# Kernel optimization log

Measured on AMD Instinct MI355X. Metric: run time of the kernel, lower is better.

Reference implementation:

```python
import jax, jax.numpy as jnp
import numpy as np

FACTOR = 5

def setup_inputs() -> dict:
    key = jax.random.key(0)
    kq, kk, kv, ki = jax.random.split(key, 4)
    B, L, H, D = 8, 2048, 8, 64
    u = FACTOR * int(np.ceil(np.log(L)))  # sample_k == n_top == 40
    return {
        "queries": jax.random.normal(kq, (B, L, H, D), dtype=jnp.float32),
        "keys": jax.random.normal(kk, (B, L, H, D), dtype=jnp.float32),
        "values": jax.random.normal(kv, (B, L, H, D), dtype=jnp.float32),
        "index_sample": jax.random.randint(ki, (L, u), 0, L, dtype=jnp.int32),
    }

def reference(queries, keys, values, index_sample):
    B, L, H, D = queries.shape
    # faithful to torch .view(B, H, -1, D) on contiguous tensors (a reshape, not a transpose)
    q = queries.reshape(B, H, L, D)
    k = keys.reshape(B, H, L, D)
    v = values.reshape(B, H, L, D)
    u = FACTOR * int(np.ceil(np.log(L)))  # U_part == u
    # --- _prob_QK: sample keys per query, score, pick top-u queries ---
    K_sample = k[:, :, index_sample, :]                      # [B,H,L,u,D] gather over L_K
    QK_sample = jnp.einsum('bhld,bhlsd->bhls', q, K_sample)  # [B,H,L,u]
    M = QK_sample.max(axis=-1) - QK_sample.sum(axis=-1) / L  # sparsity measure [B,H,L]
    M_top = jax.lax.top_k(M, u)[1]                           # [B,H,u] indices of active queries
    Q_reduce = jnp.take_along_axis(q, M_top[..., None], axis=2)  # [B,H,u,D]
    scores = jnp.einsum('bhud,bhld->bhul', Q_reduce, k)      # [B,H,u,L]
    scale = 1.0 / float(np.sqrt(D))
    attn = jax.nn.softmax(scores * scale, axis=-1)           # dropout is identity in eval
    context = jnp.einsum('bhul,bhld->bhud', attn, v)         # [B,H,u,D]
    return context, attn
```

## Files before the change

kernel.cpp:

```cpp
#include <hip/hip_runtime.h>
#include <math.h>

#define LSEQ 2048
#define DDIM 64
#define UU   40
#define NBH  64
#define NCHUNK 8
#define CROWS  256
#define CTX_ELEMS (NBH*UU*DDIM)

__device__ __forceinline__ float grp8_sum(float x) {
  float t;
  t = __int_as_float(__builtin_amdgcn_update_dpp(0, __float_as_int(x), 0xB1, 0xF, 0xF, false));
  x += t;
  t = __int_as_float(__builtin_amdgcn_update_dpp(0, __float_as_int(x), 0x4E, 0xF, 0xF, false));
  x += t;
  t = __int_as_float(__builtin_amdgcn_update_dpp(0, __float_as_int(x), 0x141, 0xF, 0xF, false));
  x += t;
  return x;
}

__global__ __launch_bounds__(256) void k0_sort(
    const int* __restrict__ idxs, int* __restrict__ sidx, int* __restrict__ soff) {
  int l = blockIdx.x * 4 + (threadIdx.x >> 6);
  int lane = threadIdx.x & 63;
  int v = 0, c = NCHUNK;
  if (lane < UU) { v = idxs[l * UU + lane]; c = v >> 8; }
  unsigned long long lower = (1ull << lane) - 1ull;
  int base = 0;
#pragma unroll
  for (int cc = 0; cc < NCHUNK; ++cc) {
    unsigned long long m = __ballot(c == cc);
    if (c == cc) {
      int rank = __popcll(m & lower);
      sidx[l * UU + base + rank] = v;
    }
    int cnt = __popcll(m);
    if (lane == cc) soff[l * NCHUNK + cc] = (base << 8) | cnt;
    base += cnt;
  }
}

__global__ __launch_bounds__(512, 4) void k12_gather(
    const float* __restrict__ q, const float* __restrict__ k,
    const int* __restrict__ sidx, const int* __restrict__ soff,
    float2* __restrict__ Mpart) {
  __shared__ float4 kt[CROWS * 16];
  int b = blockIdx.x;
  int bh = b & 63;
  int c  = b >> 6;
  int t  = threadIdx.x;

  {
    const float4* src = (const float4*)(k + ((size_t)bh * LSEQ + c * CROWS) * DDIM);
#pragma unroll
    for (int j = 0; j < 8; ++j) {
      int i = t + 512 * j;
      int row = i >> 4, col = i & 15;
      kt[row * 16 + (col ^ (row & 7))] = src[i];
    }
  }
  __syncthreads();

  int w = t >> 6;
  int lane = t & 63;
  int g = lane >> 3;
  int sub = lane & 7;

  for (int lb = 0; lb < 256; lb += 8) {
    int l = w * 256 + lb + g;
    const float4* qr = (const float4*)(q + ((size_t)bh * LSEQ + l) * DDIM);
    float4 qa = qr[sub];
    float4 qb = qr[sub + 8];
    int oc   = soff[l * NCHUNK + c];
    int cnt  = oc & 255;
    int base = oc >> 8;
    int rowv[8];
#pragma unroll
    for (int s = 0; s < 8; ++s) {
      int ix = base + s; ix = ix < UU ? ix : UU - 1;
      rowv[s] = sidx[l * UU + ix] & (CROWS - 1);
    }
    float mx = -INFINITY, sm = 0.f;
#pragma unroll
    for (int s = 0; s < 8; ++s) {
      if (s < cnt) {
        int row = rowv[s];
        int sl = (sub ^ (row & 7));
        float4 a  = kt[row * 16 + sl];
        float4 bq = kt[row * 16 + 8 + sl];
        float d = qa.x * a.x + qa.y * a.y + qa.z * a.z + qa.w * a.w
                + qb.x * bq.x + qb.y * bq.y + qb.z * bq.z + qb.w * bq.w;
        d = grp8_sum(d);
        mx = fmaxf(mx, d);
        sm += d;
      }
    }
    for (int s = 8; s < cnt; ++s) {
      int row = sidx[l * UU + base + s] & (CROWS - 1);
      int sl = (sub ^ (row & 7));
      float4 a  = kt[row * 16 + sl];
      float4 bq = kt[row * 16 + 8 + sl];
      float d = qa.x * a.x + qa.y * a.y + qa.z * a.z + qa.w * a.w
              + qb.x * bq.x + qb.y * bq.y + qb.z * bq.z + qb.w * bq.w;
      d = grp8_sum(d);
      mx = fmaxf(mx, d);
      sm += d;
    }
    if (sub == 0) Mpart[((size_t)bh * NCHUNK + c) * LSEQ + l] = make_float2(mx, sm);
  }
}

__global__ __launch_bounds__(256) void k3_topk(const float2* __restrict__ Mp,
                                               int* __restrict__ Mtop) {
  int bh = blockIdx.x;
  int t = threadIdx.x;
  int w = t >> 6;
  int lane = t & 63;
  float v[8];
#pragma unroll
  for (int j = 0; j < 8; ++j) {
    int l = t + 256 * j;
    float mxv = -INFINITY, smv = 0.f;
#pragma unroll
    for (int c = 0; c < NCHUNK; ++c) {
      float2 p = Mp[((size_t)bh * NCHUNK + c) * LSEQ + l];
      mxv = fmaxf(mxv, p.x);
      smv += p.y;
    }
    v[j] = mxv - smv * (1.0f / (float)LSEQ);
  }
  __shared__ float swv[4];
  __shared__ int   swi[4];
  __shared__ int   win;
  for (int it = 0; it < UU; ++it) {
    float bv = -INFINITY; int bi = 0x7fffffff;
#pragma unroll
    for (int j = 0; j < 8; ++j) {
      if (v[j] > bv) { bv = v[j]; bi = t + 256 * j; }
    }
#pragma unroll
    for (int off = 32; off > 0; off >>= 1) {
      float ov = __shfl_xor(bv, off, 64);
      int   oi = __shfl_xor(bi, off, 64);
      if (ov > bv || (ov == bv && oi < bi)) { bv = ov; bi = oi; }
    }
    if (lane == 0) { swv[w] = bv; swi[w] = bi; }
    __syncthreads();
    if (t == 0) {
      float fv = swv[0]; int fi = swi[0];
#pragma unroll
      for (int j = 1; j < 4; ++j) {
        if (swv[j] > fv || (swv[j] == fv && swi[j] < fi)) { fv = swv[j]; fi = swi[j]; }
      }
      Mtop[bh * UU + it] = fi;
      win = fi;
    }
    __syncthreads();
    int wi = win;
#pragma unroll
    for (int j = 0; j < 8; ++j)
      if (wi == t + 256 * j) v[j] = -INFINITY;
  }
}

__global__ __launch_bounds__(256, 4) void k45_scores_softmax(
    const float* __restrict__ q, const float* __restrict__ k,
    const int* __restrict__ Mtop, float* __restrict__ attn,
    float* __restrict__ ctx) {
  __shared__ float sct[4 * LSEQ];
  int b = blockIdx.x;
  int bh = b & 63;
  int u0 = (b >> 6) * 4;
  int t = threadIdx.x;
  int g = t >> 2;
  int sub = t & 3;

  ctx[b * 256 + t] = 0.f;

  float4 qv[4][4];
#pragma unroll
  for (int u = 0; u < 4; ++u) {
    int qi = Mtop[bh * UU + u0 + u];
    const float4* qr = (const float4*)(q + (size_t)(bh * LSEQ + qi) * DDIM);
#pragma unroll
    for (int m = 0; m < 4; ++m) qv[u][m] = qr[4 * m + sub];
  }

  const float* kb = k + (size_t)bh * LSEQ * DDIM;
#pragma unroll 1
  for (int p = 0; p < 32; ++p) {
    int l = p * 64 + g;
    const float4* kr = (const float4*)(kb + (size_t)l * DDIM);
    float4 ks[4];
#pragma unroll
    for (int m = 0; m < 4; ++m) ks[m] = kr[4 * m + sub];
    float d[4];
#pragma unroll
    for (int u = 0; u < 4; ++u) {
      float s = 0.f;
#pragma unroll
      for (int m = 0; m < 4; ++m) {
        float4 x = qv[u][m], a = ks[m];
        s += x.x * a.x + x.y * a.y + x.z * a.z + x.w * a.w;
      }
      s += __shfl_xor(s, 1, 64);
      s += __shfl_xor(s, 2, 64);
      d[u] = s * 0.125f;
    }
    if (sub == 0) {
#pragma unroll
      for (int u = 0; u < 4; ++u) sct[u * LSEQ + l] = d[u];
    }
  }
  __syncthreads();

  int w = t >> 6, lane = t & 63;
  float* row = sct + w * LSEQ;
  float vv[32];
  float mx = -INFINITY;
#pragma unroll
  for (int j = 0; j < 32; ++j) { vv[j] = row[lane + 64 * j]; mx = fmaxf(mx, vv[j]); }
#pragma unroll
  for (int off = 32; off > 0; off >>= 1) mx = fmaxf(mx, __shfl_xor(mx, off, 64));
  float sm = 0.f;
#pragma unroll
  for (int j = 0; j < 32; ++j) { vv[j] = __expf(vv[j] - mx); sm += vv[j]; }
#pragma unroll
  for (int off = 32; off > 0; off >>= 1) sm += __shfl_xor(sm, off, 64);
  float inv = 1.0f / sm;
  float* ap = attn + (size_t)(bh * UU + u0 + w) * LSEQ;
#pragma unroll
  for (int j = 0; j < 32; ++j) ap[lane + 64 * j] = vv[j] * inv;
}

__global__ __launch_bounds__(256) void k7_context(
    const float* __restrict__ attn, const float* __restrict__ v,
    float* __restrict__ ctx) {
  __shared__ float vt[256 * DDIM];
  int b = blockIdx.x;
  int bh = b & 63;
  int l0 = (b >> 6) * 256;
  int t = threadIdx.x;

  const float4* src = (const float4*)(v + ((size_t)bh * LSEQ + l0) * DDIM);
  float4* dst = (float4*)vt;
#pragma unroll
  for (int i = 0; i < 16; ++i) dst[t + 256 * i] = src[t + 256 * i];
  __syncthreads();

  int w = t >> 6;
  int d = t & 63;
  const float* ab = attn + ((size_t)bh * UU + w * 10) * LSEQ + l0;
  float acc[10];
#pragma unroll
  for (int u = 0; u < 10; ++u) acc[u] = 0.f;
#pragma unroll 1
  for (int l4 = 0; l4 < 64; ++l4) {
    int l = l4 * 4;
    float4 av[10];
#pragma unroll
    for (int u = 0; u < 10; ++u)
      av[u] = *(const float4*)(ab + (size_t)u * LSEQ + l);
#pragma unroll
    for (int i = 0; i < 4; ++i) {
      float vvv = vt[(l + i) * DDIM + d];
#pragma unroll
      for (int u = 0; u < 10; ++u)
        acc[u] = fmaf(((const float*)&av[u])[i], vvv, acc[u]);
    }
  }
#pragma unroll
  for (int u = 0; u < 10; ++u)
    atomicAdd(&ctx[((size_t)bh * UU + w * 10 + u) * DDIM + d], acc[u]);
}

extern "C" void kernel_launch(void* const* d_in, const int* in_sizes, int n_in,
                              void* d_out, int out_size, void* d_ws, size_t ws_size,
                              hipStream_t stream) {
  const float* q   = (const float*)d_in[0];
  const float* k   = (const float*)d_in[1];
  const float* v   = (const float*)d_in[2];
  const int*   idx = (const int*)d_in[3];

  float* ctx  = (float*)d_out;
  float* attn = (float*)d_out + CTX_ELEMS;
  float2* Mpart = (float2*)attn;

  int* sidx = (int*)d_ws;
  int* soff = sidx + LSEQ * UU;
  int* Mtop = soff + LSEQ * NCHUNK;

  k0_sort<<<LSEQ / 4, 256, 0, stream>>>(idx, sidx, soff);
  k12_gather<<<NBH * NCHUNK, 512, 0, stream>>>(q, k, sidx, soff, Mpart);
  k3_topk<<<NBH, 256, 0, stream>>>(Mpart, Mtop);
  k45_scores_softmax<<<NBH * 10, 256, 0, stream>>>(q, k, Mtop, attn, ctx);
  k7_context<<<NBH * 8, 256, 0, stream>>>(attn, v, ctx);
}
```

Measured before the change: 301.4 us.

## Fuse scores, softmax and context kernels, keeping attention in LDS

Merges the scores/softmax kernel with the context kernel. Each block keeps its 4 normalized attention rows in shared memory and streams V through a swizzled LDS tile to compute the context directly. This drops one launch, the re-read of attention from global memory and the ctx atomics, and the final per-row sum is done through shared memory. In exchange, each of the 640 blocks now reads the whole V for its head instead of a 256-row slice, giving about 10x total V traffic, and the launch bound drops from 4 to 3 blocks per SM.

New measurement: 290.5 us. -3.6%, faster.

```diff
diff --git a/kernel.cpp b/kernel.cpp
--- a/kernel.cpp
+++ b/kernel.cpp
@@ -164,115 +164,140 @@
   }
 }
 
-__global__ __launch_bounds__(256, 4) void k45_scores_softmax(
+__global__ __launch_bounds__(256, 3) void k457_fused(
     const float* __restrict__ q, const float* __restrict__ k,
-    const int* __restrict__ Mtop, float* __restrict__ attn,
-    float* __restrict__ ctx) {
-  __shared__ float sct[4 * LSEQ];
+    const float* __restrict__ v, const int* __restrict__ Mtop,
+    float* __restrict__ attn, float* __restrict__ ctx) {
+  __shared__ float  sct[4 * LSEQ];
+  __shared__ float4 vt4[64 * 16];
   int b = blockIdx.x;
   int bh = b & 63;
   int u0 = (b >> 6) * 4;
   int t = threadIdx.x;
-  int g = t >> 2;
-  int sub = t & 3;
-
-  ctx[b * 256 + t] = 0.f;
-
-  float4 qv[4][4];
+
+  {
+    int g = t >> 2;
+    int sub = t & 3;
+    float4 qv[4][4];
+#pragma unroll
+    for (int u = 0; u < 4; ++u) {
+      int qi = Mtop[bh * UU + u0 + u];
+      const float4* qr = (const float4*)(q + (size_t)(bh * LSEQ + qi) * DDIM);
+#pragma unroll
+      for (int m = 0; m < 4; ++m) qv[u][m] = qr[4 * m + sub];
+    }
+    const float* kb = k + (size_t)bh * LSEQ * DDIM;
+#pragma unroll 1
+    for (int p = 0; p < 32; ++p) {
+      int l = p * 64 + g;
+      const float4* kr = (const float4*)(kb + (size_t)l * DDIM);
+      float4 ks[4];
+#pragma unroll
+      for (int m = 0; m < 4; ++m) ks[m] = kr[4 * m + sub];
+      float d[4];
+#pragma unroll
+      for (int u = 0; u < 4; ++u) {
+        float s = 0.f;
+#pragma unroll
+        for (int m = 0; m < 4; ++m) {
+          float4 x = qv[u][m], a = ks[m];
+          s += x.x * a.x + x.y * a.y + x.z * a.z + x.w * a.w;
+        }
+        s += __shfl_xor(s, 1, 64);
+        s += __shfl_xor(s, 2, 64);
+        d[u] = s * 0.125f;
+      }
+      if (sub == 0) {
+#pragma unroll
+        for (int u = 0; u < 4; ++u) sct[u * LSEQ + l] = d[u];
+      }
+    }
+  }
+  __syncthreads();
+
+  int w = t >> 6, lane = t & 63;
+  {
+    float* row = sct + w * LSEQ;
+    float vv[32];
+    float mx = -INFINITY;
+#pragma unroll
+    for (int j = 0; j < 32; ++j) { vv[j] = row[lane + 64 * j]; mx = fmaxf(mx, vv[j]); }
+#pragma unroll
+    for (int off = 32; off > 0; off >>= 1) mx = fmaxf(mx, __shfl_xor(mx, off, 64));
+    float sm = 0.f;
+#pragma unroll
+    for (int j = 0; j < 32; ++j) { vv[j] = __expf(vv[j] - mx); sm += vv[j]; }
+#pragma unroll
+    for (int off = 32; off > 0; off >>= 1) sm += __shfl_xor(sm, off, 64);
+    float inv = 1.0f / sm;
+    float* ap = attn + (size_t)(bh * UU + u0 + w) * LSEQ;
+#pragma unroll
+    for (int j = 0; j < 32; ++j) {
+      float a = vv[j] * inv;
+      row[lane + 64 * j] = a;
+      ap[lane + 64 * j] = a;
+    }
+  }
+  __syncthreads();
+
+  int dq = lane & 15;
+  int lq = lane >> 4;
+  float4 acc[4];
+#pragma unroll
+  for (int u = 0; u < 4; ++u) acc[u] = make_float4(0.f, 0.f, 0.f, 0.f);
+
+  const float4* vsrc = (const float4*)(v + (size_t)bh * LSEQ * DDIM);
+#pragma unroll 1
+  for (int tile = 0; tile < 32; ++tile) {
+#pragma unroll
+    for (int i = 0; i < 4; ++i) {
+      int idx = t + 256 * i;
+      int row = idx >> 4, c4 = idx & 15;
+      vt4[row * 16 + (c4 ^ (row & 3))] = vsrc[tile * 1024 + idx];
+    }
+    __syncthreads();
+#pragma unroll
+    for (int i = 0; i < 4; ++i) {
+      int r = w * 16 + i * 4 + lq;
+      int l = tile * 64 + r;
+      float4 vv4 = vt4[r * 16 + (dq ^ (r & 3))];
+#pragma unroll
+      for (int u = 0; u < 4; ++u) {
+        float a = sct[u * LSEQ + l];
+        acc[u].x += a * vv4.x;
+        acc[u].y += a * vv4.y;
+        acc[u].z += a * vv4.z;
+        acc[u].w += a * vv4.w;
+      }
+    }
+    __syncthreads();
+  }
+
 #pragma unroll
   for (int u = 0; u < 4; ++u) {
-    int qi = Mtop[bh * UU + u0 + u];
-    const float4* qr = (const float4*)(q + (size_t)(bh * LSEQ + qi) * DDIM);
-#pragma unroll
-    for (int m = 0; m < 4; ++m) qv[u][m] = qr[4 * m + sub];
-  }
-
-  const float* kb = k + (size_t)bh * LSEQ * DDIM;
-#pragma unroll 1
-  for (int p = 0; p < 32; ++p) {
-    int l = p * 64 + g;
-    const float4* kr = (const float4*)(kb + (size_t)l * DDIM);
-    float4 ks[4];
-#pragma unroll
-    for (int m = 0; m < 4; ++m) ks[m] = kr[4 * m + sub];
-    float d[4];
-#pragma unroll
-    for (int u = 0; u < 4; ++u) {
-      float s = 0.f;
-#pragma unroll
-      for (int m = 0; m < 4; ++m) {
-        float4 x = qv[u][m], a = ks[m];
-        s += x.x * a.x + x.y * a.y + x.z * a.z + x.w * a.w;
-      }
-      s += __shfl_xor(s, 1, 64);
-      s += __shfl_xor(s, 2, 64);
-      d[u] = s * 0.125f;
-    }
-    if (sub == 0) {
-#pragma unroll
-      for (int u = 0; u < 4; ++u) sct[u * LSEQ + l] = d[u];
-    }
-  }
-  __syncthreads();
-
-  int w = t >> 6, lane = t & 63;
-  float* row = sct + w * LSEQ;
-  float vv[32];
-  float mx = -INFINITY;
-#pragma unroll
-  for (int j = 0; j < 32; ++j) { vv[j] = row[lane + 64 * j]; mx = fmaxf(mx, vv[j]); }
-#pragma unroll
-  for (int off = 32; off > 0; off >>= 1) mx = fmaxf(mx, __shfl_xor(mx, off, 64));
-  float sm = 0.f;
-#pragma unroll
-  for (int j = 0; j < 32; ++j) { vv[j] = __expf(vv[j] - mx); sm += vv[j]; }
-#pragma unroll
-  for (int off = 32; off > 0; off >>= 1) sm += __shfl_xor(sm, off, 64);
-  float inv = 1.0f / sm;
-  float* ap = attn + (size_t)(bh * UU + u0 + w) * LSEQ;
-#pragma unroll
-  for (int j = 0; j < 32; ++j) ap[lane + 64 * j] = vv[j] * inv;
-}
-
-__global__ __launch_bounds__(256) void k7_context(
-    const float* __restrict__ attn, const float* __restrict__ v,
-    float* __restrict__ ctx) {
-  __shared__ float vt[256 * DDIM];
-  int b = blockIdx.x;
-  int bh = b & 63;
-  int l0 = (b >> 6) * 256;
-  int t = threadIdx.x;
-
-  const float4* src = (const float4*)(v + ((size_t)bh * LSEQ + l0) * DDIM);
-  float4* dst = (float4*)vt;
-#pragma unroll
-  for (int i = 0; i < 16; ++i) dst[t + 256 * i] = src[t + 256 * i];
-  __syncthreads();
-
-  int w = t >> 6;
-  int d = t & 63;
-  const float* ab = attn + ((size_t)bh * UU + w * 10) * LSEQ + l0;
-  float acc[10];
-#pragma unroll
-  for (int u = 0; u < 10; ++u) acc[u] = 0.f;
-#pragma unroll 1
-  for (int l4 = 0; l4 < 64; ++l4) {
-    int l = l4 * 4;
-    float4 av[10];
-#pragma unroll
-    for (int u = 0; u < 10; ++u)
-      av[u] = *(const float4*)(ab + (size_t)u * LSEQ + l);
-#pragma unroll
-    for (int i = 0; i < 4; ++i) {
-      float vvv = vt[(l + i) * DDIM + d];
-#pragma unroll
-      for (int u = 0; u < 10; ++u)
-        acc[u] = fmaf(((const float*)&av[u])[i], vvv, acc[u]);
-    }
-  }
-#pragma unroll
-  for (int u = 0; u < 10; ++u)
-    atomicAdd(&ctx[((size_t)bh * UU + w * 10 + u) * DDIM + d], acc[u]);
+    acc[u].x += __shfl_xor(acc[u].x, 16, 64);
+    acc[u].y += __shfl_xor(acc[u].y, 16, 64);
+    acc[u].z += __shfl_xor(acc[u].z, 16, 64);
+    acc[u].w += __shfl_xor(acc[u].w, 16, 64);
+    acc[u].x += __shfl_xor(acc[u].x, 32, 64);
+    acc[u].y += __shfl_xor(acc[u].y, 32, 64);
+    acc[u].z += __shfl_xor(acc[u].z, 32, 64);
+    acc[u].w += __shfl_xor(acc[u].w, 32, 64);
+  }
+  __syncthreads();
+  float* pacc = (float*)vt4;
+  if (lq == 0) {
+#pragma unroll
+    for (int u = 0; u < 4; ++u)
+      ((float4*)pacc)[(w * 4 + u) * 16 + dq] = acc[u];
+  }
+  __syncthreads();
+  {
+    int uu = t >> 6, d = t & 63;
+    float s = pacc[(0 * 4 + uu) * 64 + d] + pacc[(1 * 4 + uu) * 64 + d]
+            + pacc[(2 * 4 + uu) * 64 + d] + pacc[(3 * 4 + uu) * 64 + d];
+    ctx[((size_t)bh * UU + u0 + uu) * DDIM + d] = s;
+  }
 }
 
 extern "C" void kernel_launch(void* const* d_in, const int* in_sizes, int n_in,
@@ -294,6 +319,5 @@
   k0_sort<<<LSEQ / 4, 256, 0, stream>>>(idx, sidx, soff);
   k12_gather<<<NBH * NCHUNK, 512, 0, stream>>>(q, k, sidx, soff, Mpart);
   k3_topk<<<NBH, 256, 0, stream>>>(Mpart, Mtop);
-  k45_scores_softmax<<<NBH * 10, 256, 0, stream>>>(q, k, Mtop, attn, ctx);
-  k7_context<<<NBH * 8, 256, 0, stream>>>(attn, v, ctx);
-}
+  k457_fused<<<NBH * 10, 256, 0, stream>>>(q, k, v, Mtop, attn, ctx);
+}
```
